# Kernel tuning notes

Measured on AMD Instinct MI355X. Metric: run time of the kernel, lower is better.

## Reference

```python
import jax, jax.numpy as jnp
import numpy as np

H, DK, DV, BS = 8, 64, 64, 128


def setup_inputs() -> dict:
    key = jax.random.key(0)
    ks = jax.random.split(key, 6)
    B, T, D = 2, 8193, 1024
    inner = H * DK
    x = jax.random.normal(ks[0], (B, T, D), jnp.float32)
    s = 0.02
    Wq = jax.random.normal(ks[1], (D, inner), jnp.float32) * s
    Wk = jax.random.normal(ks[2], (D, inner), jnp.float32) * s
    Wv = jax.random.normal(ks[3], (D, H * DV), jnp.float32) * s
    Wo = jax.random.normal(ks[4], (H * DV, D), jnp.float32) * s
    bo = jnp.zeros((D,), jnp.float32)
    return {"x": x, "Wq": Wq, "Wk": Wk, "Wv": Wv, "Wo": Wo, "bo": bo}


def _bigbird(x, Wq, Wk, Wv, Wo, bo):
    B, T, D = x.shape
    N = T - 1
    nb = N // BS
    scale = 1.0 / jnp.sqrt(jnp.asarray(DK, x.dtype))
    # projections -> (B, H, T, d)
    q = (x @ Wq).reshape(B, T, H, DK).transpose(0, 2, 1, 3)
    k = (x @ Wk).reshape(B, T, H, DK).transpose(0, 2, 1, 3)
    v = (x @ Wv).reshape(B, T, H, DV).transpose(0, 2, 1, 3)

    # global token (position 0) attends to everything
    sg = jnp.einsum('bhd,bhtd->bht', q[:, :, 0], k) * scale
    pg = jax.nn.softmax(sg, axis=-1)
    out_g = jnp.einsum('bht,bhtd->bhd', pg, v)  # (B,H,DV)

    kg = k[:, :, 0]  # (B,H,DK)
    vg = v[:, :, 0]  # (B,H,DV)
    qx = q[:, :, 1:].reshape(B, H, nb, BS, DK)
    kx = k[:, :, 1:].reshape(B, H, nb, BS, DK)
    vx = v[:, :, 1:].reshape(B, H, nb, BS, DV)

    # zero-pad one block on each side (faithful to original: zero blocks, not masked)
    kp = jnp.pad(kx, ((0, 0), (0, 0), (1, 1), (0, 0), (0, 0)))
    vp = jnp.pad(vx, ((0, 0), (0, 0), (1, 1), (0, 0), (0, 0)))
    k_local = jnp.concatenate([kp[:, :, 0:nb], kp[:, :, 1:nb + 1], kp[:, :, 2:nb + 2]], axis=3)
    v_local = jnp.concatenate([vp[:, :, 0:nb], vp[:, :, 1:nb + 1], vp[:, :, 2:nb + 2]], axis=3)

    kg_e = jnp.broadcast_to(kg[:, :, None, None, :], (B, H, nb, 1, DK))
    vg_e = jnp.broadcast_to(vg[:, :, None, None, :], (B, H, nb, 1, DV))
    k_full = jnp.concatenate([kg_e, k_local], axis=3)  # (B,H,nb,1+3BS,DK)
    v_full = jnp.concatenate([vg_e, v_local], axis=3)

    scores = jnp.einsum('bhnqd,bhnkd->bhnqk', qx, k_full) * scale
    p = jax.nn.softmax(scores, axis=-1)
    out_x = jnp.einsum('bhnqk,bhnkd->bhnqd', p, v_full).reshape(B, H, N, DV)

    out = jnp.concatenate([out_g[:, :, None, :], out_x], axis=2)  # (B,H,T,DV)
    out = out.transpose(0, 2, 1, 3).reshape(B, T, H * DV)
    return out @ Wo + bo


def reference(x, Wq, Wk, Wv, Wo, bo):
    return _bigbird(x, Wq, Wk, Wv, Wo, bo)
```

## Files before the change

### kernel.cpp

```cpp
#include <hip/hip_runtime.h>
#include <hip/hip_bf16.h>

#define T_TOK 8193
#define MROWS 16386
#define NBLK  64
#define GCH   16
#define GCS   513

typedef __attribute__((ext_vector_type(8))) short bf16x8;
typedef __attribute__((ext_vector_type(4))) float f32x4;
typedef unsigned short u16;
typedef unsigned int   u32;

__device__ __forceinline__ float blo(u32 u){ return __uint_as_float(u << 16); }
__device__ __forceinline__ float bhi(u32 u){ return __uint_as_float(u & 0xffff0000u); }
__device__ __forceinline__ u16 f2b(float f){
  u32 u = __float_as_uint(f);
  u = (u + 0x7fffu + ((u >> 16) & 1u)) >> 16;
  return (u16)u;
}
__device__ __forceinline__ float b2f(u16 v){ return __uint_as_float(((u32)v) << 16); }

#define GLDS16(gsrc, ldst) \
  __builtin_amdgcn_global_load_lds((const __attribute__((address_space(1))) void*)(gsrc), \
                                   (__attribute__((address_space(3))) void*)(ldst), 16, 0, 0)

__global__ __launch_bounds__(256)
void convx(const float* __restrict__ x, u16* __restrict__ xb)
{
  const size_t i = (size_t)blockIdx.x * 256 + threadIdx.x;
  const float4* p = (const float4*)x + i * 2;
  float4 a = p[0], b = p[1];
  uint4 st;
  st.x = (u32)f2b(a.x) | ((u32)f2b(a.y) << 16);
  st.y = (u32)f2b(a.z) | ((u32)f2b(a.w) << 16);
  st.z = (u32)f2b(b.x) | ((u32)f2b(b.y) << 16);
  st.w = (u32)f2b(b.z) | ((u32)f2b(b.w) << 16);
  *(uint4*)(xb + i * 8) = st;
}

__global__ __launch_bounds__(256)
void transposeW(const float* __restrict__ B0, const float* __restrict__ B1,
                const float* __restrict__ B2, int bpart,
                u16* __restrict__ outT, int K)
{
  __shared__ float tile[64][65];
  const int n0 = blockIdx.x * 64;
  const int k0 = blockIdx.y * 64;
  const int tx = threadIdx.x & 63;
  const int ty = threadIdx.x >> 6;
  const int part = n0 / bpart;
  const float* Bm = part == 0 ? B0 : (part == 1 ? B1 : B2);
  const int bn = n0 - part * bpart;
  #pragma unroll
  for (int i = 0; i < 16; ++i) {
    int k = i * 4 + ty;
    tile[tx][k] = Bm[(size_t)(k0 + k) * bpart + bn + tx];
  }
  __syncthreads();
  #pragma unroll
  for (int i = 0; i < 16; ++i) {
    int r = i * 4 + ty;
    outT[(size_t)(n0 + r) * K + k0 + tx] = f2b(tile[r][tx]);
  }
}

template<bool OUT_F32>
__global__ __launch_bounds__(512, 2)
void gemm8(const u16* __restrict__ A, const u16* __restrict__ BT,
           void* __restrict__ Cp, const float* __restrict__ bias,
           int M, int K, int ntm, int ntn, int ldc)
{
  __shared__ u16 lds[65536];
  const int tid  = threadIdx.x;
  const int lane = tid & 63;
  const int wid  = tid >> 6;
  const int l15  = lane & 15;
  const int g    = lane >> 4;
  const int wrh  = wid >> 2;
  const int wc   = (wid & 3) * 64;
  const int bh   = (wid & 3) >> 1;
  const int wcl  = (wid & 1) * 64;

  const int nwg  = gridDim.x;
  const int orig = blockIdx.x;
  const int q8 = nwg >> 3, r8 = nwg & 7;
  const int xcd = orig & 7, loc = orig >> 3;
  const int wg = (xcd < r8 ? xcd * (q8 + 1) : r8 * (q8 + 1) + (xcd - r8) * q8) + loc;
  const int GT  = 4;
  const int gsz = GT * ntn;
  const int tg  = wg / gsz;
  const int rem = wg - tg * gsz;
  const int gt  = (ntm - tg * GT < GT) ? (ntm - tg * GT) : GT;
  const int tn  = rem / gt;
  const int tml = rem - tn * gt;
  const int bm0 = (tg * GT + tml) * 256;
  const int bn0 = tn * 256;

  f32x4 acc[8][4];
  #pragma unroll
  for (int i = 0; i < 8; ++i)
    #pragma unroll
    for (int j = 0; j < 4; ++j) { f32x4 z = {0.f,0.f,0.f,0.f}; acc[i][j] = z; }

  const int rr  = tid >> 3;
  const int gq  = (((tid & 7) ^ (rr & 7))) * 8;
  const int ldst0 = tid * 8;
  u32 aOff[2][2], bOff[2][2];
  #pragma unroll
  for (int h = 0; h < 2; ++h)
    #pragma unroll
    for (int j = 0; j < 2; ++j) {
      int ar = bm0 + h * 128 + j * 64 + rr; if (ar >= M) ar = M - 1;
      aOff[h][j] = (u32)ar * (u32)K + gq;
      bOff[h][j] = (u32)(bn0 + h * 128 + j * 64 + rr) * (u32)K + gq;
    }

#define LBASE(BUF, AB, H) (((((BUF)*2 + (AB))*2 + (H)) * 8192))
#define STAGE_A(BUF, H, KO) do { \
    GLDS16(A + aOff[H][0] + (KO), &lds[LBASE(BUF,0,H) + ldst0]); \
    GLDS16(A + aOff[H][1] + (KO), &lds[LBASE(BUF,0,H) + 4096 + ldst0]); \
  } while (0)
#define STAGE_B(BUF, H, KO) do { \
    GLDS16(BT + bOff[H][0] + (KO), &lds[LBASE(BUF,1,H) + ldst0]); \
    GLDS16(BT + bOff[H][1] + (KO), &lds[LBASE(BUF,1,H) + 4096 + ldst0]); \
  } while (0)

  int ca[2];
  ca[0] = ((0 * 4 + g) ^ (l15 & 7)) * 8;
  ca[1] = ((1 * 4 + g) ^ (l15 & 7)) * 8;

  bf16x8 bf[4][2];

#define PHASE(BUF, P, STAGE_STMT, DOVM, VMLAST) do { \
    bf16x8 af[2][2]; \
    if ((P) == 0) { \
      _Pragma("unroll") \
      for (int ni = 0; ni < 4; ++ni) { \
        bf[ni][0] = *(const bf16x8*)&lds[LBASE(BUF,1,bh) + (wcl + ni*16 + l15)*64 + ca[0]]; \
        bf[ni][1] = *(const bf16x8*)&lds[LBASE(BUF,1,bh) + (wcl + ni*16 + l15)*64 + ca[1]]; \
      } \
    } \
    _Pragma("unroll") \
    for (int mi = 0; mi < 2; ++mi) { \
      af[mi][0] = *(const bf16x8*)&lds[LBASE(BUF,0,wrh) + (((P)*2+mi)*16 + l15)*64 + ca[0]]; \
      af[mi][1] = *(const bf16x8*)&lds[LBASE(BUF,0,wrh) + (((P)*2+mi)*16 + l15)*64 + ca[1]]; \
    } \
    STAGE_STMT; \
    __builtin_amdgcn_s_barrier(); \
    __builtin_amdgcn_s_setprio(1); \
    _Pragma("unroll") \
    for (int mi = 0; mi < 2; ++mi) \
      _Pragma("unroll") \
      for (int ni = 0; ni < 4; ++ni) { \
        acc[(P)*2+mi][ni] = __builtin_amdgcn_mfma_f32_16x16x32_bf16(af[mi][0], bf[ni][0], acc[(P)*2+mi][ni], 0, 0, 0); \
        acc[(P)*2+mi][ni] = __builtin_amdgcn_mfma_f32_16x16x32_bf16(af[mi][1], bf[ni][1], acc[(P)*2+mi][ni], 0, 0, 0); \
      } \
    __builtin_amdgcn_s_setprio(0); \
    if (DOVM) { \
      if (VMLAST) asm volatile("s_waitcnt vmcnt(0)" ::: "memory"); \
      else        asm volatile("s_waitcnt vmcnt(4)" ::: "memory"); \
    } \
    __builtin_amdgcn_s_barrier(); \
  } while (0)

  STAGE_B(0, 0, 0);  STAGE_B(0, 1, 0);
  STAGE_A(0, 0, 0);  STAGE_A(0, 1, 0);
  STAGE_B(1, 0, 64); STAGE_B(1, 1, 64);
  asm volatile("s_waitcnt vmcnt(4)" ::: "memory");
  __builtin_amdgcn_s_barrier();

  const int nit = K >> 7;
  for (int it = 0; it < nit; ++it) {
    const int t2 = it << 7;
    const bool ls = (it == nit - 1);
    PHASE(0, 0, STAGE_A(1, 0, t2 + 64), false, false);
    PHASE(0, 1, STAGE_A(1, 1, t2 + 64), false, false);
    PHASE(0, 2, if (!ls) STAGE_B(0, 0, t2 + 128), false, false);
    PHASE(0, 3, if (!ls) STAGE_B(0, 1, t2 + 128), true, ls);
    PHASE(1, 0, if (!ls) STAGE_A(0, 0, t2 + 128), false, false);
    PHASE(1, 1, if (!ls) STAGE_A(0, 1, t2 + 128), false, false);
    PHASE(1, 2, if (!ls) STAGE_B(1, 0, t2 + 192), false, false);
    PHASE(1, 3, if (!ls) STAGE_B(1, 1, t2 + 192), true, ls);
  }
#undef PHASE
#undef STAGE_A
#undef STAGE_B
#undef LBASE

  #pragma unroll
  for (int mi = 0; mi < 8; ++mi) {
    #pragma unroll
    for (int r = 0; r < 4; ++r) {
      int grow = bm0 + wrh * 128 + mi * 16 + g * 4 + r;
      if (grow >= M) continue;
      #pragma unroll
      for (int ni = 0; ni < 4; ++ni) {
        int gcol  = bn0 + wc + ni * 16 + l15;
        float val = acc[mi][ni][r];
        if (OUT_F32) ((float*)Cp)[(size_t)grow * ldc + gcol] = val + bias[gcol];
        else         ((u16*)Cp)[(size_t)grow * ldc + gcol]   = f2b(val);
      }
    }
  }
}

__global__ __launch_bounds__(256)
void gsplit(const u16* __restrict__ qkv, float* __restrict__ gbuf)
{
  const int c   = blockIdx.x & 15;
  const int h   = (blockIdx.x >> 4) & 7;
  const int b   = blockIdx.x >> 7;
  const int tid = threadIdx.x;
  const int lane = tid & 63;
  const int wid  = tid >> 6;
  const int t0 = c * GCS;
  const int t1 = (t0 + GCS < T_TOK) ? (t0 + GCS) : T_TOK;
  const int nt = t1 - t0;

  __shared__ float sc[GCS];
  __shared__ float q0s[64];
  __shared__ float wredm[4], wreds[4];
  __shared__ float psum[4][64];

  const size_t base = (size_t)b * T_TOK * 1536;
  if (tid < 32) {
    u32 u = ((const u32*)(qkv + base + h * 64))[tid];
    q0s[2 * tid] = blo(u); q0s[2 * tid + 1] = bhi(u);
  }
  __syncthreads();

  float lmax = -INFINITY;
  for (int tt = tid; tt < nt; tt += 256) {
    const uint4* kp = (const uint4*)(qkv + base + (size_t)(t0 + tt) * 1536 + 512 + h * 64);
    float a = 0.f;
    #pragma unroll
    for (int q8 = 0; q8 < 8; ++q8) {
      uint4 kk = kp[q8];
      a += q0s[q8*8+0]*blo(kk.x) + q0s[q8*8+1]*bhi(kk.x)
         + q0s[q8*8+2]*blo(kk.y) + q0s[q8*8+3]*bhi(kk.y)
         + q0s[q8*8+4]*blo(kk.z) + q0s[q8*8+5]*bhi(kk.z)
         + q0s[q8*8+6]*blo(kk.w) + q0s[q8*8+7]*bhi(kk.w);
    }
    a *= 0.125f;
    sc[tt] = a;
    lmax = fmaxf(lmax, a);
  }
  for (int o = 32; o; o >>= 1) lmax = fmaxf(lmax, __shfl_xor(lmax, o, 64));
  if (lane == 0) wredm[wid] = lmax;
  __syncthreads();
  float bmax = fmaxf(fmaxf(wredm[0], wredm[1]), fmaxf(wredm[2], wredm[3]));
  float lsum = 0.f;
  for (int tt = tid; tt < nt; tt += 256) {
    float e = __expf(sc[tt] - bmax);
    sc[tt] = e;
    lsum += e;
  }
  for (int o = 32; o; o >>= 1) lsum += __shfl_xor(lsum, o, 64);
  if (lane == 0) wreds[wid] = lsum;
  __syncthreads();
  float bsum = wreds[0] + wreds[1] + wreds[2] + wreds[3];

  const int g = tid >> 6;
  const int d = tid & 63;
  float acc = 0.f;
  for (int tt = g; tt < nt; tt += 4)
    acc += sc[tt] * b2f(qkv[base + (size_t)(t0 + tt) * 1536 + 1024 + h * 64 + d]);
  psum[g][d] = acc;
  __syncthreads();

  float* rec = gbuf + ((size_t)(b * 8 + h) * GCH + c) * 66;
  if (tid < 64)
    rec[2 + tid] = psum[0][tid] + psum[1][tid] + psum[2][tid] + psum[3][tid];
  if (tid == 64) { rec[0] = bmax; rec[1] = bsum; }
}

__global__ __launch_bounds__(64)
void gmerge(const float* __restrict__ gbuf, u16* __restrict__ attnb)
{
  const int bh = blockIdx.x;
  const int d  = threadIdx.x;
  const float* recs = gbuf + (size_t)bh * GCH * 66;
  float m = -INFINITY;
  #pragma unroll
  for (int c = 0; c < GCH; ++c) m = fmaxf(m, recs[c * 66]);
  float l = 0.f, o = 0.f;
  #pragma unroll
  for (int c = 0; c < GCH; ++c) {
    float e = __expf(recs[c * 66] - m);
    l += recs[c * 66 + 1] * e;
    o += recs[c * 66 + 2 + d] * e;
  }
  const int b = bh >> 3, h = bh & 7;
  attnb[(size_t)b * T_TOK * 512 + h * 64 + d] = f2b(o / l);
}

__global__ __launch_bounds__(256)
void local_attn_mfma(const u16* __restrict__ qkv, u16* __restrict__ attnb)
{
  const int bid = blockIdx.x;
  const int n = bid & 63;
  const int h = (bid >> 6) & 7;
  const int b = bid >> 9;
  const int tid  = threadIdx.x;
  const int lane = tid & 63;
  const int wid  = tid >> 6;
  const int l15  = lane & 15;
  const int g    = lane >> 4;

  __shared__ u16 K_lds[128 * 72];
  __shared__ u16 V_T[64 * 136];
  __shared__ u16 P_lds[4][32 * 72];
  __shared__ float bb[4][2][32];
  __shared__ float Kg[64], Vg[64];

  const size_t rb = (size_t)b * T_TOK;
  if (tid < 64) {
    Kg[tid] = b2f(qkv[rb * 1536 + 512 + h * 64 + tid]);
    Vg[tid] = b2f(qkv[rb * 1536 + 1024 + h * 64 + tid]);
  }

  const int q0row = 1 + n * 128 + wid * 32;
  bf16x8 qf[2][2];
  #pragma unroll
  for (int qt = 0; qt < 2; ++qt)
    #pragma unroll
    for (int kk = 0; kk < 2; ++kk)
      qf[qt][kk] = *(const bf16x8*)(qkv + (rb + q0row + qt * 16 + l15) * 1536 + h * 64 + kk * 32 + g * 8);

  __syncthreads();

  float sg[2];
  #pragma unroll
  for (int qt = 0; qt < 2; ++qt) {
    float part = 0.f;
    #pragma unroll
    for (int kk = 0; kk < 2; ++kk)
      #pragma unroll
      for (int i = 0; i < 8; ++i)
        part += b2f((u16)qf[qt][kk][i]) * Kg[kk * 32 + g * 8 + i];
    part += __shfl_xor(part, 16, 64);
    part += __shfl_xor(part, 32, 64);
    sg[qt] = part * 0.125f;
  }

  float m[2] = {-INFINITY, -INFINITY};
  float l[2] = {0.f, 0.f};
  f32x4 of[2][4];
  #pragma unroll
  for (int qt = 0; qt < 2; ++qt)
    #pragma unroll
    for (int dt = 0; dt < 4; ++dt) { f32x4 z = {0.f,0.f,0.f,0.f}; of[qt][dt] = z; }

  for (int dblk = 0; dblk < 3; ++dblk) {
    const int blk = n + dblk - 1;
    if (blk < 0 || blk >= NBLK) continue;
    const size_t krow0 = rb + 1 + (size_t)blk * 128;

    __syncthreads();
    #pragma unroll
    for (int it = 0; it < 4; ++it) {
      int c = it * 256 + tid;
      int key = c >> 3, oct = c & 7;
      *(uint4*)&K_lds[key * 72 + oct * 8] =
          *(const uint4*)(qkv + (krow0 + key) * 1536 + 512 + h * 64 + oct * 8);
    }
    #pragma unroll
    for (int it = 0; it < 2; ++it) {
      int c = it * 256 + tid;
      int kp2 = c & 63, oct = c >> 6;
      const u16* s0 = qkv + (krow0 + 2 * kp2) * 1536 + 1024 + h * 64 + oct * 8;
      uint4 va = *(const uint4*)s0;
      uint4 vb4 = *(const uint4*)(s0 + 1536);
      union { uint4 q; u16 hh[8]; } ua, ub;
      ua.q = va; ub.q = vb4;
      #pragma unroll
      for (int i = 0; i < 8; ++i) {
        u32 w = (u32)ua.hh[i] | ((u32)ub.hh[i] << 16);
        *(u32*)&V_T[(oct * 8 + i) * 136 + 2 * kp2] = w;
      }
    }
    __syncthreads();

    f32x4 st[2][8];
    #pragma unroll
    for (int kt = 0; kt < 8; ++kt) {
      bf16x8 kfr[2];
      #pragma unroll
      for (int kk = 0; kk < 2; ++kk)
        kfr[kk] = *(const bf16x8*)&K_lds[(kt * 16 + l15) * 72 + kk * 32 + g * 8];
      #pragma unroll
      for (int qt = 0; qt < 2; ++qt) {
        f32x4 z = {0.f,0.f,0.f,0.f};
        z = __builtin_amdgcn_mfma_f32_16x16x32_bf16(kfr[0], qf[qt][0], z, 0, 0, 0);
        z = __builtin_amdgcn_mfma_f32_16x16x32_bf16(kfr[1], qf[qt][1], z, 0, 0, 0);
        st[qt][kt] = z;
      }
    }
    #pragma unroll
    for (int qt = 0; qt < 2; ++qt) {
      float bm = -INFINITY;
      #pragma unroll
      for (int kt = 0; kt < 8; ++kt)
        #pragma unroll
        for (int r = 0; r < 4; ++r) bm = fmaxf(bm, st[qt][kt][r]);
      bm = fmaxf(bm, __shfl_xor(bm, 16, 64));
      bm = fmaxf(bm, __shfl_xor(bm, 32, 64));
      bm *= 0.125f;
      float mn = fmaxf(m[qt], bm);
      float corr = __expf(m[qt] - mn);
      float bsum = 0.f;
      #pragma unroll
      for (int kt = 0; kt < 8; ++kt)
        #pragma unroll
        for (int r = 0; r < 4; ++r) {
          float p = __expf(__builtin_fmaf(st[qt][kt][r], 0.125f, -mn));
          st[qt][kt][r] = p;
          bsum += p;
        }
      bsum += __shfl_xor(bsum, 16, 64);
      bsum += __shfl_xor(bsum, 32, 64);
      l[qt] = l[qt] * corr + bsum;
      m[qt] = mn;
      if (lane < 16) bb[wid][0][qt * 16 + lane] = corr;
    }
    float rc[2][4];
    #pragma unroll
    for (int qt = 0; qt < 2; ++qt)
      #pragma unroll
      for (int r = 0; r < 4; ++r) rc[qt][r] = bb[wid][0][qt * 16 + g * 4 + r];
    #pragma unroll
    for (int qt = 0; qt < 2; ++qt)
      #pragma unroll
      for (int dt = 0; dt < 4; ++dt)
        #pragma unroll
        for (int r = 0; r < 4; ++r) of[qt][dt][r] *= rc[qt][r];

    u16* P_w = (u16*)P_lds[wid];
    #pragma unroll
    for (int half = 0; half < 2; ++half) {
      #pragma unroll
      for (int qt = 0; qt < 2; ++qt)
        #pragma unroll
        for (int k4 = 0; k4 < 4; ++k4) {
          int kt = half * 4 + k4;
          u16 h0 = f2b(st[qt][kt][0]), h1 = f2b(st[qt][kt][1]);
          u16 h2 = f2b(st[qt][kt][2]), h3 = f2b(st[qt][kt][3]);
          uint2 pk = { (u32)h0 | ((u32)h1 << 16), (u32)h2 | ((u32)h3 << 16) };
          *(uint2*)&P_w[(qt * 16 + l15) * 72 + k4 * 16 + g * 4] = pk;
        }
      #pragma unroll
      for (int ks = 0; ks < 2; ++ks) {
        bf16x8 pa[2];
        #pragma unroll
        for (int qt = 0; qt < 2; ++qt)
          pa[qt] = *(const bf16x8*)&P_w[(qt * 16 + l15) * 72 + ks * 32 + g * 8];
        #pragma unroll
        for (int dt = 0; dt < 4; ++dt) {
          bf16x8 vb = *(const bf16x8*)&V_T[(dt * 16 + l15) * 136 + half * 64 + ks * 32 + g * 8];
          #pragma unroll
          for (int qt = 0; qt < 2; ++qt)
            of[qt][dt] = __builtin_amdgcn_mfma_f32_16x16x32_bf16(pa[qt], vb, of[qt][dt], 0, 0, 0);
        }
      }
    }
  }

  const int nz = (n == 0) + (n == NBLK - 1);
  #pragma unroll
  for (int qt = 0; qt < 2; ++qt) {
    float mf   = fmaxf(m[qt], sg[qt]);
    float corr = __expf(m[qt] - mf);
    float eg   = __expf(sg[qt] - mf);
    float lf   = l[qt] * corr + eg;
    if (nz) lf += (float)(nz * 128) * __expf(-mf);
    float inv = 1.f / lf;
    if (lane < 16) {
      bb[wid][0][qt * 16 + lane] = corr * inv;
      bb[wid][1][qt * 16 + lane] = eg * inv;
    }
  }
  float vgr[4];
  #pragma unroll
  for (int dt = 0; dt < 4; ++dt) vgr[dt] = Vg[dt * 16 + l15];
  #pragma unroll
  for (int qt = 0; qt < 2; ++qt)
    #pragma unroll
    for (int r = 0; r < 4; ++r) {
      float af = bb[wid][0][qt * 16 + g * 4 + r];
      float bf = bb[wid][1][qt * 16 + g * 4 + r];
      int row = q0row + qt * 16 + g * 4 + r;
      u16* dst = attnb + (rb + row) * 512 + h * 64;
      #pragma unroll
      for (int dt = 0; dt < 4; ++dt)
        dst[dt * 16 + l15] = f2b(of[qt][dt][r] * af + bf * vgr[dt]);
    }
}

extern "C" void kernel_launch(void* const* d_in, const int* in_sizes, int n_in,
                              void* d_out, int out_size, void* d_ws, size_t ws_size,
                              hipStream_t stream) {
  (void)in_sizes; (void)n_in; (void)out_size; (void)ws_size;
  const float* x  = (const float*)d_in[0];
  const float* Wq = (const float*)d_in[1];
  const float* Wk = (const float*)d_in[2];
  const float* Wv = (const float*)d_in[3];
  const float* Wo = (const float*)d_in[4];
  const float* bo = (const float*)d_in[5];
  float* out = (float*)d_out;

  char* ws = (char*)d_ws;
  u16* qkv   = (u16*)ws;
  u16* xb    = (u16*)(ws + 50337792);
  u16* attnb = (u16*)(ws + 50337792);
  u16* WoT   = (u16*)(ws + 67117056);
  u16* WqkvT = (u16*)d_out;
  float* gbuf = (float*)((char*)d_out + (4 << 20));

  dim3 blk(256);
  convx<<<dim3(8193), blk, 0, stream>>>(x, xb);
  transposeW<<<dim3(24, 16), blk, 0, stream>>>(Wq, Wk, Wv, 512, WqkvT, 1024);
  gemm8<false><<<dim3(65 * 6), dim3(512), 0, stream>>>(xb, WqkvT, qkv, nullptr, MROWS, 1024, 65, 6, 1536);
  transposeW<<<dim3(16, 8), blk, 0, stream>>>(Wo, Wo, Wo, 1024, WoT, 512);
  gsplit<<<dim3(256), blk, 0, stream>>>(qkv, gbuf);
  gmerge<<<dim3(16), dim3(64), 0, stream>>>(gbuf, attnb);
  local_attn_mfma<<<dim3(1024), blk, 0, stream>>>(qkv, attnb);
  gemm8<true><<<dim3(65 * 4), dim3(512), 0, stream>>>(attnb, WoT, out, bo, MROWS, 512, 65, 4, 1024);
}
```

Measured before the change: 205.1 us.

## Split GEMM tail rows into a separate small kernel and drop bounds checks

The two projection GEMMs now launch only the 64 full 256-row tiles (16384 rows), removing the partially filled 65th tile row and the per-row bounds clamps and checks. The two leftover rows go to a new small dot-product kernel. The single shared buffer is also split into four named LDS arrays. This trims wasted MFMA work on the mostly empty tile and the branch overhead, at the cost of two extra small launches.

```diff
diff --git a/kernel.cpp b/kernel.cpp
--- a/kernel.cpp
+++ b/kernel.cpp
@@ -3,6 +3,7 @@
 
 #define T_TOK 8193
 #define MROWS 16386
+#define M_MAIN 16384
 #define NBLK  64
 #define GCH   16
 #define GCS   513
@@ -66,12 +67,40 @@
 }
 
 template<bool OUT_F32>
+__global__ __launch_bounds__(256)
+void tail_rows(const u16* __restrict__ A, const u16* __restrict__ BT,
+               void* __restrict__ Cp, const float* __restrict__ bias,
+               int K, int ldc)
+{
+  __shared__ u16 arow[1024];
+  const int row = M_MAIN + blockIdx.y;
+  const int col = blockIdx.x * 256 + threadIdx.x;
+  for (int i = threadIdx.x; i < K; i += 256)
+    arow[i] = A[(size_t)row * K + i];
+  __syncthreads();
+  const u16* bp = BT + (size_t)col * K;
+  float acc = 0.f;
+  for (int k = 0; k < K; k += 8) {
+    uint4 u = *(const uint4*)(bp + k);
+    acc += b2f(arow[k+0]) * blo(u.x) + b2f(arow[k+1]) * bhi(u.x)
+         + b2f(arow[k+2]) * blo(u.y) + b2f(arow[k+3]) * bhi(u.y)
+         + b2f(arow[k+4]) * blo(u.z) + b2f(arow[k+5]) * bhi(u.z)
+         + b2f(arow[k+6]) * blo(u.w) + b2f(arow[k+7]) * bhi(u.w);
+  }
+  if (OUT_F32) ((float*)Cp)[(size_t)row * ldc + col] = acc + bias[col];
+  else         ((u16*)Cp)[(size_t)row * ldc + col]   = f2b(acc);
+}
+
+template<bool OUT_F32>
 __global__ __launch_bounds__(512, 2)
 void gemm8(const u16* __restrict__ A, const u16* __restrict__ BT,
            void* __restrict__ Cp, const float* __restrict__ bias,
-           int M, int K, int ntm, int ntn, int ldc)
-{
-  __shared__ u16 lds[65536];
+           int K, int ntm, int ntn, int ldc)
+{
+  __shared__ u16 As0[16384];
+  __shared__ u16 As1[16384];
+  __shared__ u16 Bs0[16384];
+  __shared__ u16 Bs1[16384];
   const int tid  = threadIdx.x;
   const int lane = tid & 63;
   const int wid  = tid >> 6;
@@ -104,47 +133,44 @@
     for (int j = 0; j < 4; ++j) { f32x4 z = {0.f,0.f,0.f,0.f}; acc[i][j] = z; }
 
   const int rr  = tid >> 3;
-  const int gq  = (((tid & 7) ^ (rr & 7))) * 8;
+  const int gq  = ((tid & 7) ^ (rr & 7)) * 8;
   const int ldst0 = tid * 8;
   u32 aOff[2][2], bOff[2][2];
   #pragma unroll
   for (int h = 0; h < 2; ++h)
     #pragma unroll
     for (int j = 0; j < 2; ++j) {
-      int ar = bm0 + h * 128 + j * 64 + rr; if (ar >= M) ar = M - 1;
-      aOff[h][j] = (u32)ar * (u32)K + gq;
+      aOff[h][j] = (u32)(bm0 + h * 128 + j * 64 + rr) * (u32)K + gq;
       bOff[h][j] = (u32)(bn0 + h * 128 + j * 64 + rr) * (u32)K + gq;
     }
 
-#define LBASE(BUF, AB, H) (((((BUF)*2 + (AB))*2 + (H)) * 8192))
-#define STAGE_A(BUF, H, KO) do { \
-    GLDS16(A + aOff[H][0] + (KO), &lds[LBASE(BUF,0,H) + ldst0]); \
-    GLDS16(A + aOff[H][1] + (KO), &lds[LBASE(BUF,0,H) + 4096 + ldst0]); \
+#define STAGE_A(ARR, H, KO) do { \
+    GLDS16(A + aOff[H][0] + (KO), &ARR[(H) * 8192 + ldst0]); \
+    GLDS16(A + aOff[H][1] + (KO), &ARR[(H) * 8192 + 4096 + ldst0]); \
   } while (0)
-#define STAGE_B(BUF, H, KO) do { \
-    GLDS16(BT + bOff[H][0] + (KO), &lds[LBASE(BUF,1,H) + ldst0]); \
-    GLDS16(BT + bOff[H][1] + (KO), &lds[LBASE(BUF,1,H) + 4096 + ldst0]); \
+#define STAGE_B(ARR, H, KO) do { \
+    GLDS16(BT + bOff[H][0] + (KO), &ARR[(H) * 8192 + ldst0]); \
+    GLDS16(BT + bOff[H][1] + (KO), &ARR[(H) * 8192 + 4096 + ldst0]); \
   } while (0)
 
-  int ca[2];
-  ca[0] = ((0 * 4 + g) ^ (l15 & 7)) * 8;
-  ca[1] = ((1 * 4 + g) ^ (l15 & 7)) * 8;
-
-  bf16x8 bf[4][2];
-
-#define PHASE(BUF, P, STAGE_STMT, DOVM, VMLAST) do { \
+  const int ca0 = (g ^ (l15 & 7)) * 8;
+  const int ca1 = ((4 + g) ^ (l15 & 7)) * 8;
+
+  bf16x8 bfr[4][2];
+
+#define PHASE(AARR, BARR, P, STAGE_STMT, DOVM, VMLAST) do { \
     bf16x8 af[2][2]; \
     if ((P) == 0) { \
       _Pragma("unroll") \
       for (int ni = 0; ni < 4; ++ni) { \
-        bf[ni][0] = *(const bf16x8*)&lds[LBASE(BUF,1,bh) + (wcl + ni*16 + l15)*64 + ca[0]]; \
-        bf[ni][1] = *(const bf16x8*)&lds[LBASE(BUF,1,bh) + (wcl + ni*16 + l15)*64 + ca[1]]; \
+        bfr[ni][0] = *(const bf16x8*)&BARR[bh * 8192 + (wcl + ni*16 + l15)*64 + ca0]; \
+        bfr[ni][1] = *(const bf16x8*)&BARR[bh * 8192 + (wcl + ni*16 + l15)*64 + ca1]; \
       } \
     } \
     _Pragma("unroll") \
     for (int mi = 0; mi < 2; ++mi) { \
-      af[mi][0] = *(const bf16x8*)&lds[LBASE(BUF,0,wrh) + (((P)*2+mi)*16 + l15)*64 + ca[0]]; \
-      af[mi][1] = *(const bf16x8*)&lds[LBASE(BUF,0,wrh) + (((P)*2+mi)*16 + l15)*64 + ca[1]]; \
+      af[mi][0] = *(const bf16x8*)&AARR[wrh * 8192 + (((P)*2+mi)*16 + l15)*64 + ca0]; \
+      af[mi][1] = *(const bf16x8*)&AARR[wrh * 8192 + (((P)*2+mi)*16 + l15)*64 + ca1]; \
     } \
     STAGE_STMT; \
     __builtin_amdgcn_s_barrier(); \
@@ -153,8 +179,8 @@
     for (int mi = 0; mi < 2; ++mi) \
       _Pragma("unroll") \
       for (int ni = 0; ni < 4; ++ni) { \
-        acc[(P)*2+mi][ni] = __builtin_amdgcn_mfma_f32_16x16x32_bf16(af[mi][0], bf[ni][0], acc[(P)*2+mi][ni], 0, 0, 0); \
-        acc[(P)*2+mi][ni] = __builtin_amdgcn_mfma_f32_16x16x32_bf16(af[mi][1], bf[ni][1], acc[(P)*2+mi][ni], 0, 0, 0); \
+        acc[(P)*2+mi][ni] = __builtin_amdgcn_mfma_f32_16x16x32_bf16(af[mi][0], bfr[ni][0], acc[(P)*2+mi][ni], 0, 0, 0); \
+        acc[(P)*2+mi][ni] = __builtin_amdgcn_mfma_f32_16x16x32_bf16(af[mi][1], bfr[ni][1], acc[(P)*2+mi][ni], 0, 0, 0); \
       } \
     __builtin_amdgcn_s_setprio(0); \
     if (DOVM) { \
@@ -164,9 +190,9 @@
     __builtin_amdgcn_s_barrier(); \
   } while (0)
 
-  STAGE_B(0, 0, 0);  STAGE_B(0, 1, 0);
-  STAGE_A(0, 0, 0);  STAGE_A(0, 1, 0);
-  STAGE_B(1, 0, 64); STAGE_B(1, 1, 64);
+  STAGE_B(Bs0, 0, 0);  STAGE_B(Bs0, 1, 0);
+  STAGE_A(As0, 0, 0);  STAGE_A(As0, 1, 0);
+  STAGE_B(Bs1, 0, 64); STAGE_B(Bs1, 1, 64);
   asm volatile("s_waitcnt vmcnt(4)" ::: "memory");
   __builtin_amdgcn_s_barrier();
 
@@ -174,26 +200,24 @@
   for (int it = 0; it < nit; ++it) {
     const int t2 = it << 7;
     const bool ls = (it == nit - 1);
-    PHASE(0, 0, STAGE_A(1, 0, t2 + 64), false, false);
-    PHASE(0, 1, STAGE_A(1, 1, t2 + 64), false, false);
-    PHASE(0, 2, if (!ls) STAGE_B(0, 0, t2 + 128), false, false);
-    PHASE(0, 3, if (!ls) STAGE_B(0, 1, t2 + 128), true, ls);
-    PHASE(1, 0, if (!ls) STAGE_A(0, 0, t2 + 128), false, false);
-    PHASE(1, 1, if (!ls) STAGE_A(0, 1, t2 + 128), false, false);
-    PHASE(1, 2, if (!ls) STAGE_B(1, 0, t2 + 192), false, false);
-    PHASE(1, 3, if (!ls) STAGE_B(1, 1, t2 + 192), true, ls);
+    PHASE(As0, Bs0, 0, STAGE_A(As1, 0, t2 + 64), false, false);
+    PHASE(As0, Bs0, 1, STAGE_A(As1, 1, t2 + 64), false, false);
+    PHASE(As0, Bs0, 2, if (!ls) STAGE_B(Bs0, 0, t2 + 128), false, false);
+    PHASE(As0, Bs0, 3, if (!ls) STAGE_B(Bs0, 1, t2 + 128), true, ls);
+    PHASE(As1, Bs1, 0, if (!ls) STAGE_A(As0, 0, t2 + 128), false, false);
+    PHASE(As1, Bs1, 1, if (!ls) STAGE_A(As0, 1, t2 + 128), false, false);
+    PHASE(As1, Bs1, 2, if (!ls) STAGE_B(Bs1, 0, t2 + 192), false, false);
+    PHASE(As1, Bs1, 3, if (!ls) STAGE_B(Bs1, 1, t2 + 192), true, ls);
   }
 #undef PHASE
 #undef STAGE_A
 #undef STAGE_B
-#undef LBASE
 
   #pragma unroll
   for (int mi = 0; mi < 8; ++mi) {
     #pragma unroll
     for (int r = 0; r < 4; ++r) {
       int grow = bm0 + wrh * 128 + mi * 16 + g * 4 + r;
-      if (grow >= M) continue;
       #pragma unroll
       for (int ni = 0; ni < 4; ++ni) {
         int gcol  = bn0 + wc + ni * 16 + l15;
@@ -520,10 +544,12 @@
   dim3 blk(256);
   convx<<<dim3(8193), blk, 0, stream>>>(x, xb);
   transposeW<<<dim3(24, 16), blk, 0, stream>>>(Wq, Wk, Wv, 512, WqkvT, 1024);
-  gemm8<false><<<dim3(65 * 6), dim3(512), 0, stream>>>(xb, WqkvT, qkv, nullptr, MROWS, 1024, 65, 6, 1536);
+  gemm8<false><<<dim3(64 * 6), dim3(512), 0, stream>>>(xb, WqkvT, qkv, nullptr, 1024, 64, 6, 1536);
+  tail_rows<false><<<dim3(6, 2), blk, 0, stream>>>(xb, WqkvT, qkv, nullptr, 1024, 1536);
   transposeW<<<dim3(16, 8), blk, 0, stream>>>(Wo, Wo, Wo, 1024, WoT, 512);
   gsplit<<<dim3(256), blk, 0, stream>>>(qkv, gbuf);
   gmerge<<<dim3(16), dim3(64), 0, stream>>>(gbuf, attnb);
   local_attn_mfma<<<dim3(1024), blk, 0, stream>>>(qkv, attnb);
-  gemm8<true><<<dim3(65 * 4), dim3(512), 0, stream>>>(attnb, WoT, out, bo, MROWS, 512, 65, 4, 1024);
-}
+  gemm8<true><<<dim3(64 * 4), dim3(512), 0, stream>>>(attnb, WoT, out, bo, 512, 64, 4, 1024);
+  tail_rows<true><<<dim3(4, 2), blk, 0, stream>>>(attnb, WoT, out, bo, 512, 1024);
+}
```

After: 224.9 us. 9.7% more time.

## Fuse fp32-to-bf16 conversion of x into the QKV projection GEMM

Applied to the files above, without the earlier changes.

Drops the separate convx kernel and adds gemm8f, which reads fp32 x directly, converts it to bf16 in registers, and writes it swizzled into LDS. B tiles still stream through global_load_lds DMA. This removes a full write and re-read of the bf16 copy of x (about 33 MB of extra traffic) and one kernel launch. In exchange the GEMM reads twice the A bytes per tile, uses register-staged A loads with hand-tuned waitcnts, and drops to one workgroup per CU, so it may lose latency hiding.

```diff
diff --git a/kernel.cpp b/kernel.cpp
--- a/kernel.cpp
+++ b/kernel.cpp
@@ -20,24 +20,13 @@
   return (u16)u;
 }
 __device__ __forceinline__ float b2f(u16 v){ return __uint_as_float(((u32)v) << 16); }
+__device__ __forceinline__ u32 pk2(float a, float b){
+  return (u32)f2b(a) | ((u32)f2b(b) << 16);
+}
 
 #define GLDS16(gsrc, ldst) \
   __builtin_amdgcn_global_load_lds((const __attribute__((address_space(1))) void*)(gsrc), \
                                    (__attribute__((address_space(3))) void*)(ldst), 16, 0, 0)
-
-__global__ __launch_bounds__(256)
-void convx(const float* __restrict__ x, u16* __restrict__ xb)
-{
-  const size_t i = (size_t)blockIdx.x * 256 + threadIdx.x;
-  const float4* p = (const float4*)x + i * 2;
-  float4 a = p[0], b = p[1];
-  uint4 st;
-  st.x = (u32)f2b(a.x) | ((u32)f2b(a.y) << 16);
-  st.y = (u32)f2b(a.z) | ((u32)f2b(a.w) << 16);
-  st.z = (u32)f2b(b.x) | ((u32)f2b(b.y) << 16);
-  st.w = (u32)f2b(b.z) | ((u32)f2b(b.w) << 16);
-  *(uint4*)(xb + i * 8) = st;
-}
 
 __global__ __launch_bounds__(256)
 void transposeW(const float* __restrict__ B0, const float* __restrict__ B1,
@@ -62,6 +51,191 @@
   for (int i = 0; i < 16; ++i) {
     int r = i * 4 + ty;
     outT[(size_t)(n0 + r) * K + k0 + tx] = f2b(tile[r][tx]);
+  }
+}
+
+__global__ __launch_bounds__(512, 1)
+void gemm8f(const float* __restrict__ X, const u16* __restrict__ BT,
+            u16* __restrict__ C, int M, int K, int ntm, int ntn, int ldc)
+{
+  __shared__ u16 As0[16384];
+  __shared__ u16 As1[16384];
+  __shared__ u16 Bs0[16384];
+  __shared__ u16 Bs1[16384];
+  const int tid  = threadIdx.x;
+  const int lane = tid & 63;
+  const int wid  = tid >> 6;
+  const int l15  = lane & 15;
+  const int g    = lane >> 4;
+  const int wrh  = wid >> 2;
+  const int wc   = (wid & 3) * 64;
+  const int bh   = (wid & 3) >> 1;
+  const int wcl  = (wid & 1) * 64;
+
+  const int nwg  = gridDim.x;
+  const int orig = blockIdx.x;
+  const int q8 = nwg >> 3, r8 = nwg & 7;
+  const int xcd = orig & 7, loc = orig >> 3;
+  const int wg = (xcd < r8 ? xcd * (q8 + 1) : r8 * (q8 + 1) + (xcd - r8) * q8) + loc;
+  const int GT  = 4;
+  const int gsz = GT * ntn;
+  const int tg  = wg / gsz;
+  const int rem = wg - tg * gsz;
+  const int gt  = (ntm - tg * GT < GT) ? (ntm - tg * GT) : GT;
+  const int tn  = rem / gt;
+  const int tml = rem - tn * gt;
+  const int bm0 = (tg * GT + tml) * 256;
+  const int bn0 = tn * 256;
+
+  f32x4 acc[8][4];
+  #pragma unroll
+  for (int i = 0; i < 8; ++i)
+    #pragma unroll
+    for (int j = 0; j < 4; ++j) { f32x4 z = {0.f,0.f,0.f,0.f}; acc[i][j] = z; }
+
+  const int rr = tid >> 3;
+  const int ch = tid & 7;
+  const float* ax[2][2];
+  int wofs[2][2];
+  #pragma unroll
+  for (int H = 0; H < 2; ++H)
+    #pragma unroll
+    for (int j = 0; j < 2; ++j) {
+      int ar = bm0 + H * 128 + j * 64 + rr; if (ar >= M) ar = M - 1;
+      ax[H][j]   = X + (size_t)ar * K + ch * 8;
+      wofs[H][j] = H * 8192 + (j * 64 + rr) * 64 + ((ch ^ (rr & 7)) * 8);
+    }
+  const int gq = ((ch ^ (rr & 7))) * 8;
+  u32 bOff[2][2];
+  #pragma unroll
+  for (int h = 0; h < 2; ++h)
+    #pragma unroll
+    for (int j = 0; j < 2; ++j)
+      bOff[h][j] = (u32)(bn0 + h * 128 + j * 64 + rr) * (u32)K + gq;
+  const int ldst0 = tid * 8;
+
+#define B_DMA(ARR, KO) do { \
+    GLDS16(BT + bOff[0][0] + (KO), &ARR[ldst0]); \
+    GLDS16(BT + bOff[0][1] + (KO), &ARR[4096 + ldst0]); \
+    GLDS16(BT + bOff[1][0] + (KO), &ARR[8192 + ldst0]); \
+    GLDS16(BT + bOff[1][1] + (KO), &ARR[8192 + 4096 + ldst0]); \
+  } while (0)
+#define A_ISSUE(DST, KO) do { \
+    _Pragma("unroll") for (int H = 0; H < 2; ++H) \
+      _Pragma("unroll") for (int j = 0; j < 2; ++j) { \
+        DST[H][j][0] = *(const float4*)(ax[H][j] + (KO)); \
+        DST[H][j][1] = *(const float4*)(ax[H][j] + (KO) + 4); } \
+  } while (0)
+#define A_WRITE(ARR, SRC) do { \
+    _Pragma("unroll") for (int H = 0; H < 2; ++H) \
+      _Pragma("unroll") for (int j = 0; j < 2; ++j) { \
+        uint4 w; \
+        w.x = pk2(SRC[H][j][0].x, SRC[H][j][0].y); \
+        w.y = pk2(SRC[H][j][0].z, SRC[H][j][0].w); \
+        w.z = pk2(SRC[H][j][1].x, SRC[H][j][1].y); \
+        w.w = pk2(SRC[H][j][1].z, SRC[H][j][1].w); \
+        *(uint4*)&ARR[wofs[H][j]] = w; } \
+  } while (0)
+
+  const int ca0 = (g ^ (l15 & 7)) * 8;
+  const int ca1 = ((4 + g) ^ (l15 & 7)) * 8;
+  bf16x8 bfr[4][2];
+  float4 fa[2][2][2];
+
+#define RD_A(ARR, P) { \
+    _Pragma("unroll") for (int mi = 0; mi < 2; ++mi) { \
+      af[mi][0] = *(const bf16x8*)&ARR[wrh * 8192 + (((P)*2+mi)*16 + l15)*64 + ca0]; \
+      af[mi][1] = *(const bf16x8*)&ARR[wrh * 8192 + (((P)*2+mi)*16 + l15)*64 + ca1]; } }
+#define RD_B(ARR) { \
+    _Pragma("unroll") for (int ni = 0; ni < 4; ++ni) { \
+      bfr[ni][0] = *(const bf16x8*)&ARR[bh * 8192 + (wcl + ni*16 + l15)*64 + ca0]; \
+      bfr[ni][1] = *(const bf16x8*)&ARR[bh * 8192 + (wcl + ni*16 + l15)*64 + ca1]; } }
+#define MFMA_PH(P) { \
+    __builtin_amdgcn_s_barrier(); \
+    __builtin_amdgcn_s_setprio(1); \
+    _Pragma("unroll") for (int mi = 0; mi < 2; ++mi) \
+      _Pragma("unroll") for (int ni = 0; ni < 4; ++ni) { \
+        acc[(P)*2+mi][ni] = __builtin_amdgcn_mfma_f32_16x16x32_bf16(af[mi][0], bfr[ni][0], acc[(P)*2+mi][ni], 0, 0, 0); \
+        acc[(P)*2+mi][ni] = __builtin_amdgcn_mfma_f32_16x16x32_bf16(af[mi][1], bfr[ni][1], acc[(P)*2+mi][ni], 0, 0, 0); } \
+    __builtin_amdgcn_s_setprio(0); }
+
+  {
+    float4 pa[2][2][2];
+    A_ISSUE(pa, 0);
+    asm volatile("" ::: "memory");
+    B_DMA(Bs0, 0);
+    asm volatile("" ::: "memory");
+    A_ISSUE(fa, 64);
+    asm volatile("" ::: "memory");
+    B_DMA(Bs1, 64);
+    asm volatile("s_waitcnt vmcnt(12)" ::: "memory");
+    A_WRITE(As0, pa);
+    asm volatile("s_waitcnt lgkmcnt(0)" ::: "memory");
+    __builtin_amdgcn_s_barrier();
+  }
+
+  const int nit = K >> 7;
+  for (int it = 0; it < nit; ++it) {
+    const int ko = it << 7;
+    const bool ls = (it == nit - 1);
+    bf16x8 af[2][2];
+    asm volatile("s_waitcnt vmcnt(4)" ::: "memory");
+    A_WRITE(As1, fa);
+    __builtin_amdgcn_sched_barrier(0);
+    RD_B(Bs0); RD_A(As0, 0);
+    if (!ls) A_ISSUE(fa, ko + 128);
+    asm volatile("s_waitcnt lgkmcnt(12)" ::: "memory");
+    MFMA_PH(0);
+    __builtin_amdgcn_s_barrier();
+    RD_A(As0, 1);
+    MFMA_PH(1);
+    __builtin_amdgcn_s_barrier();
+    RD_A(As0, 2);
+    if (!ls) B_DMA(Bs0, ko + 128);
+    MFMA_PH(2);
+    __builtin_amdgcn_s_barrier();
+    RD_A(As0, 3);
+    MFMA_PH(3);
+    if (ls) asm volatile("s_waitcnt vmcnt(0)" ::: "memory");
+    else    asm volatile("s_waitcnt vmcnt(4)" ::: "memory");
+    __builtin_amdgcn_s_barrier();
+    if (!ls) { A_WRITE(As0, fa); __builtin_amdgcn_sched_barrier(0); }
+    RD_B(Bs1); RD_A(As1, 0);
+    asm volatile("s_waitcnt lgkmcnt(12)" ::: "memory");
+    MFMA_PH(0);
+    __builtin_amdgcn_s_barrier();
+    RD_A(As1, 1);
+    if (!ls) { A_ISSUE(fa, ko + 192); asm volatile("" ::: "memory"); }
+    MFMA_PH(1);
+    __builtin_amdgcn_s_barrier();
+    RD_A(As1, 2);
+    if (!ls) B_DMA(Bs1, ko + 192);
+    MFMA_PH(2);
+    __builtin_amdgcn_s_barrier();
+    RD_A(As1, 3);
+    MFMA_PH(3);
+    if (!ls) asm volatile("s_waitcnt vmcnt(12)" ::: "memory");
+    __builtin_amdgcn_s_barrier();
+  }
+#undef RD_A
+#undef RD_B
+#undef MFMA_PH
+#undef B_DMA
+#undef A_ISSUE
+#undef A_WRITE
+
+  #pragma unroll
+  for (int mi = 0; mi < 8; ++mi) {
+    #pragma unroll
+    for (int r = 0; r < 4; ++r) {
+      int grow = bm0 + wrh * 128 + mi * 16 + g * 4 + r;
+      if (grow >= M) continue;
+      #pragma unroll
+      for (int ni = 0; ni < 4; ++ni) {
+        int gcol = bn0 + wc + ni * 16 + l15;
+        C[(size_t)grow * ldc + gcol] = f2b(acc[mi][ni][r]);
+      }
+    }
   }
 }
 
@@ -104,7 +278,7 @@
     for (int j = 0; j < 4; ++j) { f32x4 z = {0.f,0.f,0.f,0.f}; acc[i][j] = z; }
 
   const int rr  = tid >> 3;
-  const int gq  = (((tid & 7) ^ (rr & 7))) * 8;
+  const int gq  = ((tid & 7) ^ (rr & 7)) * 8;
   const int ldst0 = tid * 8;
   u32 aOff[2][2], bOff[2][2];
   #pragma unroll
@@ -126,25 +300,24 @@
     GLDS16(BT + bOff[H][1] + (KO), &lds[LBASE(BUF,1,H) + 4096 + ldst0]); \
   } while (0)
 
-  int ca[2];
-  ca[0] = ((0 * 4 + g) ^ (l15 & 7)) * 8;
-  ca[1] = ((1 * 4 + g) ^ (l15 & 7)) * 8;
-
-  bf16x8 bf[4][2];
+  const int ca0 = (g ^ (l15 & 7)) * 8;
+  const int ca1 = ((4 + g) ^ (l15 & 7)) * 8;
+
+  bf16x8 bfr[4][2];
 
 #define PHASE(BUF, P, STAGE_STMT, DOVM, VMLAST) do { \
     bf16x8 af[2][2]; \
     if ((P) == 0) { \
       _Pragma("unroll") \
       for (int ni = 0; ni < 4; ++ni) { \
-        bf[ni][0] = *(const bf16x8*)&lds[LBASE(BUF,1,bh) + (wcl + ni*16 + l15)*64 + ca[0]]; \
-        bf[ni][1] = *(const bf16x8*)&lds[LBASE(BUF,1,bh) + (wcl + ni*16 + l15)*64 + ca[1]]; \
+        bfr[ni][0] = *(const bf16x8*)&lds[LBASE(BUF,1,bh) + (wcl + ni*16 + l15)*64 + ca0]; \
+        bfr[ni][1] = *(const bf16x8*)&lds[LBASE(BUF,1,bh) + (wcl + ni*16 + l15)*64 + ca1]; \
       } \
     } \
     _Pragma("unroll") \
     for (int mi = 0; mi < 2; ++mi) { \
-      af[mi][0] = *(const bf16x8*)&lds[LBASE(BUF,0,wrh) + (((P)*2+mi)*16 + l15)*64 + ca[0]]; \
-      af[mi][1] = *(const bf16x8*)&lds[LBASE(BUF,0,wrh) + (((P)*2+mi)*16 + l15)*64 + ca[1]]; \
+      af[mi][0] = *(const bf16x8*)&lds[LBASE(BUF,0,wrh) + (((P)*2+mi)*16 + l15)*64 + ca0]; \
+      af[mi][1] = *(const bf16x8*)&lds[LBASE(BUF,0,wrh) + (((P)*2+mi)*16 + l15)*64 + ca1]; \
     } \
     STAGE_STMT; \
     __builtin_amdgcn_s_barrier(); \
@@ -153,8 +326,8 @@
     for (int mi = 0; mi < 2; ++mi) \
       _Pragma("unroll") \
       for (int ni = 0; ni < 4; ++ni) { \
-        acc[(P)*2+mi][ni] = __builtin_amdgcn_mfma_f32_16x16x32_bf16(af[mi][0], bf[ni][0], acc[(P)*2+mi][ni], 0, 0, 0); \
-        acc[(P)*2+mi][ni] = __builtin_amdgcn_mfma_f32_16x16x32_bf16(af[mi][1], bf[ni][1], acc[(P)*2+mi][ni], 0, 0, 0); \
+        acc[(P)*2+mi][ni] = __builtin_amdgcn_mfma_f32_16x16x32_bf16(af[mi][0], bfr[ni][0], acc[(P)*2+mi][ni], 0, 0, 0); \
+        acc[(P)*2+mi][ni] = __builtin_amdgcn_mfma_f32_16x16x32_bf16(af[mi][1], bfr[ni][1], acc[(P)*2+mi][ni], 0, 0, 0); \
       } \
     __builtin_amdgcn_s_setprio(0); \
     if (DOVM) { \
@@ -511,16 +684,14 @@
 
   char* ws = (char*)d_ws;
   u16* qkv   = (u16*)ws;
-  u16* xb    = (u16*)(ws + 50337792);
   u16* attnb = (u16*)(ws + 50337792);
   u16* WoT   = (u16*)(ws + 67117056);
   u16* WqkvT = (u16*)d_out;
   float* gbuf = (float*)((char*)d_out + (4 << 20));
 
   dim3 blk(256);
-  convx<<<dim3(8193), blk, 0, stream>>>(x, xb);
   transposeW<<<dim3(24, 16), blk, 0, stream>>>(Wq, Wk, Wv, 512, WqkvT, 1024);
-  gemm8<false><<<dim3(65 * 6), dim3(512), 0, stream>>>(xb, WqkvT, qkv, nullptr, MROWS, 1024, 65, 6, 1536);
+  gemm8f<<<dim3(65 * 6), dim3(512), 0, stream>>>(x, WqkvT, qkv, MROWS, 1024, 65, 6, 1536);
   transposeW<<<dim3(16, 8), blk, 0, stream>>>(Wo, Wo, Wo, 1024, WoT, 512);
   gsplit<<<dim3(256), blk, 0, stream>>>(qkv, gbuf);
   gmerge<<<dim3(16), dim3(64), 0, stream>>>(gbuf, attnb);
```

Result: slower. 240.8 us (+17.4%).
